# Optimization experiments

Measured on AMD Instinct MI355X. Metric: run time of the kernel, lower is better.

Reference implementation:

```python
import jax, jax.numpy as jnp
import numpy as np

N_NODES = 100000


def _gcn_norm(edge_index, num_nodes):
    # PyG gcn_norm with add_self_loops=True, edge_weight=1:
    # A_hat = A + I; norm_e = deg^{-1/2}[src] * deg^{-1/2}[dst]
    loop = jnp.arange(num_nodes, dtype=edge_index.dtype)
    src = jnp.concatenate([edge_index[0], loop])
    dst = jnp.concatenate([edge_index[1], loop])
    deg = jax.ops.segment_sum(jnp.ones_like(src, dtype=jnp.float32), dst,
                              num_segments=num_nodes)
    dinv = jnp.where(deg > 0, jax.lax.rsqrt(deg), 0.0)
    norm = dinv[src] * dinv[dst]  # [E + N]
    return src, dst, norm


def _gcn_conv(x, src, dst, norm, W, b, num_nodes):
    h = x @ W                                  # [N, out] dense GEMM
    msg = h[src] * norm[:, None]               # gather + scale per edge
    out = jax.ops.segment_sum(msg, dst, num_segments=num_nodes)
    return out + b


def setup_inputs() -> dict:
    key = jax.random.key(0)
    k1, k2, k3, k4, k5, k6 = jax.random.split(key, 6)
    in_c, hid_c, out_c = 128, 128, 64
    E = 3200000
    x = jax.random.normal(k1, (N_NODES, in_c), dtype=jnp.float32)
    edge_index = jax.random.randint(k2, (2, E), 0, N_NODES, dtype=jnp.int64)
    # Glorot-style init for GCNConv linear weights, zero bias (PyG default)
    W1 = jax.random.normal(k3, (in_c, hid_c), dtype=jnp.float32) / np.sqrt(in_c)
    b1 = jnp.zeros((hid_c,), dtype=jnp.float32)
    W2 = jax.random.normal(k4, (hid_c, out_c), dtype=jnp.float32) / np.sqrt(hid_c)
    b2 = jnp.zeros((out_c,), dtype=jnp.float32)
    return {"x": x, "edge_index": edge_index, "W1": W1, "b1": b1,
            "W2": W2, "b2": b2}


def reference(x, edge_index, W1, b1, W2, b2):
    # Dropout is identity in eval mode (F.dropout(training=False)).
    src, dst, norm = _gcn_norm(edge_index, N_NODES)
    h = _gcn_conv(x, src, dst, norm, W1, b1, N_NODES)
    out = _gcn_conv(h, src, dst, norm, W2, b2, N_NODES)
    return out
```

## Files before the change

### kernel.cpp

```cpp
#include <hip/hip_runtime.h>
#include <hip/hip_fp16.h>
#include <cstdint>
#include <cstddef>


#define NB    391
#define BSH   8
#define CAPS  32
#define PBLK  512
#define OVCAP 4096
#define CAPB  9216

typedef _Float16 half8 __attribute__((ext_vector_type(8)));
typedef float    floatx4 __attribute__((ext_vector_type(4)));


__global__ __launch_bounds__(256) void partition_k(
    const int* __restrict__ src, const int* __restrict__ dst,
    int* __restrict__ ovcur, unsigned* __restrict__ ovrecs,
    unsigned* __restrict__ tailbuf, int* __restrict__ tailcnt, int E) {
    __shared__ unsigned stag[NB][CAPS + 1];
    __shared__ int scnt[NB];
    const int t = threadIdx.x;
    for (int i = t; i < NB; i += 256) scnt[i] = 0;
    __syncthreads();

    const int Q = E >> 2;
    const int per = (Q + PBLK - 1) / PBLK;
    const int qbeg = blockIdx.x * per;
    const int qend = min(qbeg + per, Q);
    const int4* src4 = (const int4*)src;
    const int4* dst4 = (const int4*)dst;

    for (int q = qbeg + t; q < qend; q += 256) {
        const int4 s4 = src4[q];
        const int4 d4 = dst4[q];
#pragma unroll
        for (int j = 0; j < 4; ++j) {
            const int s = (&s4.x)[j], d = (&d4.x)[j];
            const int b = d >> BSH;
            const unsigned rec = ((unsigned)(d & 255) << 17) | (unsigned)s;
            const int slot = atomicAdd(&scnt[b], 1);
            if (slot < CAPS) stag[b][slot] = rec;
            else { const int p = atomicAdd(&ovcur[b], 1); ovrecs[(size_t)b * OVCAP + p] = rec; }
        }
    }
    if (blockIdx.x == 0) {
        for (int e = (E & ~3) + t; e < E; e += 256) {
            const int s = src[e], d = dst[e];
            const int b = d >> BSH;
            const unsigned rec = ((unsigned)(d & 255) << 17) | (unsigned)s;
            const int slot = atomicAdd(&scnt[b], 1);
            if (slot < CAPS) stag[b][slot] = rec;
            else { const int p = atomicAdd(&ovcur[b], 1); ovrecs[(size_t)b * OVCAP + p] = rec; }
        }
    }
    __syncthreads();

    for (int i = t; i < NB * CAPS; i += 256) {
        const int b = i >> 5, j = i & 31;
        if (j < min(scnt[b], CAPS))
            tailbuf[((size_t)b * PBLK + blockIdx.x) * CAPS + j] = stag[b][j];
    }
    for (int b = t; b < NB; b += 256)
        tailcnt[blockIdx.x * NB + b] = min(scnt[b], CAPS);
}

__global__ __launch_bounds__(256) void build_k(
    const unsigned* __restrict__ ovrecs, const int* __restrict__ ovcur,
    const unsigned* __restrict__ tailbuf, const int* __restrict__ tailcnt,
    int* __restrict__ rbeg, int* __restrict__ rend,
    int* __restrict__ csr, float* __restrict__ dinv, int N) {
    __shared__ int tcs[PBLK];
    __shared__ int soff[PBLK];
    __shared__ int sseg[256];
    __shared__ unsigned lrec[CAPB];
    __shared__ int cnt[256];
    __shared__ int scan[256];
    __shared__ int lpos[256];
    __shared__ int tcum_sh;
    const int t = threadIdx.x, b = blockIdx.x;
    const int n0 = b << BSH;
    const int nn = min(256, N - n0);
    const int gbase = b * CAPB;
    const size_t tb0 = (size_t)b * PBLK * CAPS;
    const int ov = ovcur[b];

    for (int i = t; i < PBLK; i += 256) tcs[i] = tailcnt[i * NB + b];
    cnt[t] = 0;
    __syncthreads();

    const int a0 = tcs[2 * t], a1 = tcs[2 * t + 1];
    sseg[t] = a0 + a1;
    __syncthreads();
    for (int o = 1; o < 256; o <<= 1) {
        int x = (t >= o) ? sseg[t - o] : 0;
        __syncthreads(); sseg[t] += x; __syncthreads();
    }
    const int ex2 = sseg[t] - (a0 + a1);
    soff[2 * t] = ex2;
    soff[2 * t + 1] = ex2 + a0;
    if (t == 255) tcum_sh = sseg[255];
    __syncthreads();
    const int tcum = tcum_sh;

    for (int i = t; i < PBLK * CAPS; i += 256) {
        const int seg = i >> 5, j = i & 31;
        if (j < tcs[seg]) lrec[soff[seg] + j] = tailbuf[tb0 + i];
    }
    for (int i = t; i < ov; i += 256) lrec[tcum + i] = ovrecs[(size_t)b * OVCAP + i];
    __syncthreads();

    const int tot = tcum + ov;
    for (int i = t; i < tot; i += 256) atomicAdd(&cnt[lrec[i] >> 17], 1);
    __syncthreads();

    scan[t] = cnt[t];
    __syncthreads();
    for (int o = 1; o < 256; o <<= 1) {
        int x = (t >= o) ? scan[t - o] : 0;
        __syncthreads(); scan[t] += x; __syncthreads();
    }
    const int excl = scan[t] - cnt[t];
    lpos[t] = excl;
    if (t < nn) {
        rbeg[n0 + t] = gbase + excl;
        rend[n0 + t] = gbase + scan[t];
        dinv[n0 + t] = rsqrtf((float)(cnt[t] + 1));
    }
    __syncthreads();

    for (int i = t; i < tot; i += 256) {
        const unsigned r = lrec[i];
        const int pq = atomicAdd(&lpos[r >> 17], 1);
        csr[gbase + pq] = (int)(r & 0x1FFFFu);
    }
}

__global__ __launch_bounds__(256) void w12_k(
    const float* __restrict__ W1, const float* __restrict__ W2,
    const float* __restrict__ b1, _Float16* __restrict__ BhiT,
    _Float16* __restrict__ BloT, float* __restrict__ c2) {
    const int t = threadIdx.x;
    if (blockIdx.x < 32) {
        const int r = blockIdx.x * 4 + (t >> 6);
        const int c = t & 63;
        float acc = 0.f;
        for (int k = 0; k < 128; ++k) acc += W1[r * 128 + k] * W2[k * 64 + c];
        const _Float16 h = (_Float16)acc;
        BhiT[c * 128 + r] = h;
        BloT[c * 128 + r] = (_Float16)(acc - (float)h);
    } else if (t < 64) {
        float acc = 0.f;
        for (int k = 0; k < 128; ++k) acc += b1[k] * W2[k * 64 + t];
        c2[t] = acc;
    }
}

__global__ __launch_bounds__(256) void gemm_mfma_k(
    const float* __restrict__ X, const _Float16* __restrict__ BhiT,
    const _Float16* __restrict__ BloT, const float* __restrict__ dinv,
    __half* __restrict__ g, int N) {
    const int t = threadIdx.x;
    const int wave = t >> 6, lane = t & 63;
    const int m16 = lane & 15;
    const int quad = lane >> 4;
    const int rowbase = blockIdx.x * 64 + wave * 16;
    const int arow = min(rowbase + m16, N - 1);

    floatx4 acc[4] = {{0.f,0.f,0.f,0.f},{0.f,0.f,0.f,0.f},
                      {0.f,0.f,0.f,0.f},{0.f,0.f,0.f,0.f}};

#pragma unroll
    for (int ks = 0; ks < 4; ++ks) {
        const int k0 = ks * 32 + quad * 8;
        const float4 xa = *(const float4*)(X + (size_t)arow * 128 + k0);
        const float4 xb = *(const float4*)(X + (size_t)arow * 128 + k0 + 4);
        const float xs[8] = {xa.x, xa.y, xa.z, xa.w, xb.x, xb.y, xb.z, xb.w};
        half8 ahi, alo;
#pragma unroll
        for (int j = 0; j < 8; ++j) {
            const _Float16 h = (_Float16)xs[j];
            ahi[j] = h;
            alo[j] = (_Float16)(xs[j] - (float)h);
        }
#pragma unroll
        for (int c = 0; c < 4; ++c) {
            const int n = c * 16 + m16;
            const half8 bhi = *(const half8*)(BhiT + n * 128 + k0);
            const half8 blo = *(const half8*)(BloT + n * 128 + k0);
            acc[c] = __builtin_amdgcn_mfma_f32_16x16x32_f16(ahi, bhi, acc[c], 0, 0, 0);
            acc[c] = __builtin_amdgcn_mfma_f32_16x16x32_f16(ahi, blo, acc[c], 0, 0, 0);
            acc[c] = __builtin_amdgcn_mfma_f32_16x16x32_f16(alo, bhi, acc[c], 0, 0, 0);
        }
    }

#pragma unroll
    for (int r = 0; r < 4; ++r) {
        const int grow = rowbase + quad * 4 + r;
        if (grow < N) {
            const float di = dinv[grow];
#pragma unroll
            for (int c = 0; c < 4; ++c)
                g[(size_t)grow * 64 + c * 16 + m16] = __float2half(acc[c][r] * di);
        }
    }
}

template <int PASS2>
__global__ __launch_bounds__(256) void agg_k(
    const __half* __restrict__ gin, const int* __restrict__ rbeg,
    const int* __restrict__ rend, const int* __restrict__ csr,
    const float* __restrict__ dinv, void* __restrict__ outp,
    float* __restrict__ p, const float* __restrict__ c2,
    const float* __restrict__ b2, int N) {
    const int dd = (blockIdx.x * 256 + threadIdx.x) >> 6;
    const int d = __builtin_amdgcn_readfirstlane(dd);
    if (d >= N) return;
    const int lane = threadIdx.x & 63;
    const int beg = rbeg[d], end = rend[d];
    const float di = dinv[d];

    float acc = __half2float(gin[((size_t)d << 6) + lane]);
    float accp = PASS2 ? 0.f : di;

    int e = beg;
    for (; e + 16 <= end; e += 16) {
        int s[16];
#pragma unroll
        for (int j = 0; j < 16; ++j) s[j] = csr[e + j];
        float v[16];
#pragma unroll
        for (int j = 0; j < 16; ++j) v[j] = __half2float(gin[((size_t)s[j] << 6) + lane]);
        if (!PASS2) {
#pragma unroll
            for (int j = 0; j < 16; ++j) accp += dinv[s[j]];
        }
#pragma unroll
        for (int j = 0; j < 16; ++j) acc += v[j];
    }
    for (; e + 4 <= end; e += 4) {
        int s[4];
#pragma unroll
        for (int j = 0; j < 4; ++j) s[j] = csr[e + j];
        float v[4];
#pragma unroll
        for (int j = 0; j < 4; ++j) v[j] = __half2float(gin[((size_t)s[j] << 6) + lane]);
        if (!PASS2) {
#pragma unroll
            for (int j = 0; j < 4; ++j) accp += dinv[s[j]];
        }
#pragma unroll
        for (int j = 0; j < 4; ++j) acc += v[j];
    }
    for (; e < end; ++e) {
        const int s = csr[e];
        if (!PASS2) accp += dinv[s];
        acc += __half2float(gin[((size_t)s << 6) + lane]);
    }

    if (PASS2) {
        ((float*)outp)[((size_t)d << 6) + lane] = acc * di + p[d] * c2[lane] + b2[lane];
    } else {
        ((__half*)outp)[((size_t)d << 6) + lane] = __float2half(acc * di * di);
        if (lane == 0) p[d] = di * accp;
    }
}

extern "C" void kernel_launch(void* const* d_in, const int* in_sizes, int n_in,
                              void* d_out, int out_size, void* d_ws, size_t ws_size,
                              hipStream_t stream) {
    const float* x  = (const float*)d_in[0];
    const int*   ei = (const int*)d_in[1];
    const float* W1 = (const float*)d_in[2];
    const float* b1 = (const float*)d_in[3];
    const float* W2 = (const float*)d_in[4];
    const float* b2 = (const float*)d_in[5];
    float* out = (float*)d_out;

    const int N = in_sizes[0] / 128;
    const int E = in_sizes[1] / 2;
    const int* src = ei;
    const int* dst = ei + E;

    char* ws = (char*)d_ws;
    auto take = [&](size_t bytes) { char* q = ws; ws += (bytes + 255) & ~(size_t)255; return q; };
    int*      ovcur   = (int*)     take(NB * 4);
    int*      rbeg    = (int*)     take((size_t)N * 4);
    int*      rendp   = (int*)     take((size_t)N * 4);
    float*    dinv    = (float*)   take((size_t)N * 4);
    float*    pbuf    = (float*)   take((size_t)N * 4);
    _Float16* BhiT    = (_Float16*)take(128 * 64 * 2);
    _Float16* BloT    = (_Float16*)take(128 * 64 * 2);
    float*    c2      = (float*)   take(64 * 4);
    int*      tailcnt = (int*)     take((size_t)NB * PBLK * 4);
    unsigned* ovrecs  = (unsigned*)take((size_t)NB * OVCAP * 4);
    unsigned* tailbuf = (unsigned*)take((size_t)NB * PBLK * CAPS * 4);
    int*      csr     = (int*)     take((size_t)NB * CAPB * 4);
    __half*   g       = (__half*)  take((size_t)N * 64 * 2);
    __half*   t1      = (__half*)  take((size_t)N * 64 * 2);

    hipMemsetAsync(ovcur, 0, NB * 4, stream);

    partition_k<<<PBLK, 256, 0, stream>>>(src, dst, ovcur, ovrecs, tailbuf, tailcnt, E);
    build_k<<<NB, 256, 0, stream>>>(ovrecs, ovcur, tailbuf, tailcnt, rbeg, rendp, csr, dinv, N);
    w12_k<<<33, 256, 0, stream>>>(W1, W2, b1, BhiT, BloT, c2);
    gemm_mfma_k<<<(N + 63) / 64, 256, 0, stream>>>(x, BhiT, BloT, dinv, g, N);

    const int aggBlocks = (int)(((size_t)N * 64 + 255) / 256);
    agg_k<0><<<aggBlocks, 256, 0, stream>>>(g,  rbeg, rendp, csr, dinv, t1,  pbuf, c2, b2, N);
    agg_k<1><<<aggBlocks, 256, 0, stream>>>(t1, rbeg, rendp, csr, dinv, out, pbuf, c2, b2, N);
}
```

Before: 344.4 us.

## Split each node's edge list across four lane groups with vectorized half4 gathers

```diff
diff --git a/kernel.cpp b/kernel.cpp
--- a/kernel.cpp
+++ b/kernel.cpp
@@ -214,56 +214,94 @@
     const float* __restrict__ dinv, void* __restrict__ outp,
     float* __restrict__ p, const float* __restrict__ c2,
     const float* __restrict__ b2, int N) {
-    const int dd = (blockIdx.x * 256 + threadIdx.x) >> 6;
-    const int d = __builtin_amdgcn_readfirstlane(dd);
+    const int d = (blockIdx.x * 256 + threadIdx.x) >> 6;
+    const int lane = threadIdx.x & 63;
     if (d >= N) return;
-    const int lane = threadIdx.x & 63;
+    const int fo = (lane & 15) << 2;
+    const int q  = lane >> 4;
     const int beg = rbeg[d], end = rend[d];
+    const int len = end - beg;
     const float di = dinv[d];
 
-    float acc = __half2float(gin[((size_t)d << 6) + lane]);
-    float accp = PASS2 ? 0.f : di;
-
-    int e = beg;
-    for (; e + 16 <= end; e += 16) {
-        int s[16];
-#pragma unroll
-        for (int j = 0; j < 16; ++j) s[j] = csr[e + j];
-        float v[16];
-#pragma unroll
-        for (int j = 0; j < 16; ++j) v[j] = __half2float(gin[((size_t)s[j] << 6) + lane]);
-        if (!PASS2) {
-#pragma unroll
-            for (int j = 0; j < 16; ++j) accp += dinv[s[j]];
-        }
-#pragma unroll
-        for (int j = 0; j < 16; ++j) acc += v[j];
-    }
-    for (; e + 4 <= end; e += 4) {
-        int s[4];
-#pragma unroll
-        for (int j = 0; j < 4; ++j) s[j] = csr[e + j];
-        float v[4];
-#pragma unroll
-        for (int j = 0; j < 4; ++j) v[j] = __half2float(gin[((size_t)s[j] << 6) + lane]);
-        if (!PASS2) {
-#pragma unroll
-            for (int j = 0; j < 4; ++j) accp += dinv[s[j]];
-        }
-#pragma unroll
-        for (int j = 0; j < 4; ++j) acc += v[j];
-    }
-    for (; e < end; ++e) {
+    auto gat4 = [&](int s) -> float4 {
+        const uint2 w = *(const uint2*)(gin + ((size_t)s << 6) + fo);
+        const float2 a = __half22float2(*(const __half2*)&w.x);
+        const float2 b = __half22float2(*(const __half2*)&w.y);
+        return make_float4(a.x, a.y, b.x, b.y);
+    };
+
+    float4 acc = make_float4(0.f, 0.f, 0.f, 0.f);
+    float accp = 0.f;
+
+    int e        = beg + ((len * q) >> 2);
+    const int eE = beg + ((len * (q + 1)) >> 2);
+
+    while (e < eE && (e & 3)) {
+        const int s = csr[e++];
+        const float4 f = gat4(s);
+        if (!PASS2) accp += dinv[s];
+        acc.x += f.x; acc.y += f.y; acc.z += f.z; acc.w += f.w;
+    }
+    for (; e + 8 <= eE; e += 8) {
+        const int4 sa = *(const int4*)(csr + e);
+        const int4 sb = *(const int4*)(csr + e + 4);
+        const float4 f0 = gat4(sa.x), f1 = gat4(sa.y), f2 = gat4(sa.z), f3 = gat4(sa.w);
+        const float4 f4 = gat4(sb.x), f5 = gat4(sb.y), f6 = gat4(sb.z), f7 = gat4(sb.w);
+        if (!PASS2)
+            accp += ((dinv[sa.x] + dinv[sa.y]) + (dinv[sa.z] + dinv[sa.w]))
+                  + ((dinv[sb.x] + dinv[sb.y]) + (dinv[sb.z] + dinv[sb.w]));
+        acc.x += ((f0.x + f1.x) + (f2.x + f3.x)) + ((f4.x + f5.x) + (f6.x + f7.x));
+        acc.y += ((f0.y + f1.y) + (f2.y + f3.y)) + ((f4.y + f5.y) + (f6.y + f7.y));
+        acc.z += ((f0.z + f1.z) + (f2.z + f3.z)) + ((f4.z + f5.z) + (f6.z + f7.z));
+        acc.w += ((f0.w + f1.w) + (f2.w + f3.w)) + ((f4.w + f5.w) + (f6.w + f7.w));
+    }
+    if (e + 4 <= eE) {
+        const int4 sa = *(const int4*)(csr + e);
+        const float4 f0 = gat4(sa.x), f1 = gat4(sa.y), f2 = gat4(sa.z), f3 = gat4(sa.w);
+        if (!PASS2)
+            accp += (dinv[sa.x] + dinv[sa.y]) + (dinv[sa.z] + dinv[sa.w]);
+        acc.x += (f0.x + f1.x) + (f2.x + f3.x);
+        acc.y += (f0.y + f1.y) + (f2.y + f3.y);
+        acc.z += (f0.z + f1.z) + (f2.z + f3.z);
+        acc.w += (f0.w + f1.w) + (f2.w + f3.w);
+        e += 4;
+    }
+    for (; e < eE; ++e) {
         const int s = csr[e];
+        const float4 f = gat4(s);
         if (!PASS2) accp += dinv[s];
-        acc += __half2float(gin[((size_t)s << 6) + lane]);
-    }
-
-    if (PASS2) {
-        ((float*)outp)[((size_t)d << 6) + lane] = acc * di + p[d] * c2[lane] + b2[lane];
-    } else {
-        ((__half*)outp)[((size_t)d << 6) + lane] = __float2half(acc * di * di);
-        if (lane == 0) p[d] = di * accp;
+        acc.x += f.x; acc.y += f.y; acc.z += f.z; acc.w += f.w;
+    }
+
+    acc.x += __shfl_xor(acc.x, 16); acc.y += __shfl_xor(acc.y, 16);
+    acc.z += __shfl_xor(acc.z, 16); acc.w += __shfl_xor(acc.w, 16);
+    acc.x += __shfl_xor(acc.x, 32); acc.y += __shfl_xor(acc.y, 32);
+    acc.z += __shfl_xor(acc.z, 32); acc.w += __shfl_xor(acc.w, 32);
+    if (!PASS2) { accp += __shfl_xor(accp, 16); accp += __shfl_xor(accp, 32); }
+
+    if (q == 0) {
+        const float4 fs = gat4(d);
+        acc.x += fs.x; acc.y += fs.y; acc.z += fs.z; acc.w += fs.w;
+        if (PASS2) {
+            const float4 cc = *(const float4*)(c2 + fo);
+            const float4 bb = *(const float4*)(b2 + fo);
+            const float pd = p[d];
+            float4 o;
+            o.x = acc.x * di + pd * cc.x + bb.x;
+            o.y = acc.y * di + pd * cc.y + bb.y;
+            o.z = acc.z * di + pd * cc.z + bb.z;
+            o.w = acc.w * di + pd * cc.w + bb.w;
+            *(float4*)((float*)outp + ((size_t)d << 6) + fo) = o;
+        } else {
+            const float sc = di * di;
+            const __half2 h0 = __floats2half2_rn(acc.x * sc, acc.y * sc);
+            const __half2 h1 = __floats2half2_rn(acc.z * sc, acc.w * sc);
+            uint2 w;
+            w.x = *(const unsigned*)&h0;
+            w.y = *(const unsigned*)&h1;
+            *(uint2*)((__half*)outp + ((size_t)d << 6) + fo) = w;
+            if (lane == 0) p[d] = di * (di + accp);
+        }
     }
 }
 
```

Measured after the change: 408.1 us. 18.5% more time.
